# Kernel tuning notes

Hardware: AMD Instinct MI355X
Metric: run time of the kernel (lower is better)

## Reference

```python
import jax, jax.numpy as jnp
import numpy as np

BETA = 2.0  # init kwarg beta


def _roi_map(roi_params, H, W):
    # roi_params: (N, K, 4) = (mu_x, mu_y, sigma_x, sigma_y) in [0, 1]
    dtype = roi_params.dtype
    gx = (jnp.arange(W, dtype=dtype) + 0.5) / W  # x-coords of grid columns
    gy = (jnp.arange(H, dtype=dtype) + 0.5) / H  # y-coords of grid rows
    mu_x, mu_y = roi_params[:, :, 0], roi_params[:, :, 1]
    sg_x, sg_y = roi_params[:, :, 2], roi_params[:, :, 3]
    # separable generalized-Gaussian log pdf along each axis
    log_x = -(jnp.abs(gx[None, None, :] - mu_x[:, :, None]) / sg_x[:, :, None]) ** BETA  # (N,K,W)
    log_y = -(jnp.abs(gy[None, None, :] - mu_y[:, :, None]) / sg_y[:, :, None]) ** BETA  # (N,K,H)
    scores = jnp.exp(log_y[:, :, :, None] + log_x[:, :, None, :])  # (N,K,H,W)
    mx = jnp.max(scores, axis=(2, 3), keepdims=True)
    return scores / (mx + 1e-12)  # max-normalized attention maps


def setup_inputs() -> dict:
    key = jax.random.key(0)
    k1, k2 = jax.random.split(key)
    x = jax.random.normal(k1, (16, 128, 128, 256), dtype=jnp.float32)
    roi_params = jax.random.uniform(k2, (16, 64, 4), dtype=jnp.float32)
    return {"x": x, "roi_params": roi_params}


def reference(x, roi_params):
    N, H, W, d = x.shape
    roi_map = _roi_map(roi_params, H, W)           # (N,K,H,W)
    flat_map = roi_map.reshape(N, -1, H * W)        # (N,K,HW)
    flat_feats = x.reshape(N, H * W, d)             # (N,HW,d)
    roi_features = jnp.einsum('nrf,nfd->nrd', flat_map, flat_feats) / (H * W)
    return roi_features, roi_params, roi_map
```

## Files before the change

kernel.cpp:

```cpp
#include <hip/hip_runtime.h>
#include <hip/hip_bf16.h>
#include <math.h>

#define NB 16
#define RB 64
#define HB 128
#define WB 128
#define DB 256
#define HW (HB * WB)

typedef __attribute__((ext_vector_type(8))) short bf16x8;
typedef __attribute__((ext_vector_type(4))) float f32x4;

static __device__ __forceinline__ short f2bf(float f) {
  __hip_bfloat16 h = __float2bfloat16(f);
  return *reinterpret_cast<short*>(&h);
}

#define GLOAD_LDS16(gp, lp)                                          \
  __builtin_amdgcn_global_load_lds(                                  \
      (const __attribute__((address_space(1))) unsigned int*)(gp),   \
      (__attribute__((address_space(3))) unsigned int*)(lp), 16, 0, 0)

__global__ void tables_kernel(const float* __restrict__ roi,
                              float* __restrict__ ws,
                              float* __restrict__ out_params) {
  const int nr = blockIdx.x;
  const int t  = threadIdx.x;

  const float mux = roi[nr * 4 + 0];
  const float muy = roi[nr * 4 + 1];
  const float sgx = roi[nr * 4 + 2];
  const float sgy = roi[nr * 4 + 3];

  const float g  = (t + 0.5f) * (1.0f / 128.0f);
  const float tx = fabsf(g - mux) / sgx;
  const float ty = fabsf(g - muy) / sgy;
  const float lx = -(tx * tx);
  const float ly = -(ty * ty);

  __shared__ float sdx[128], sdy[128];
  sdx[t] = lx; sdy[t] = ly;
  __syncthreads();
  for (int off = 64; off > 0; off >>= 1) {
    if (t < off) {
      sdx[t] = fmaxf(sdx[t], sdx[t + off]);
      sdy[t] = fmaxf(sdy[t], sdy[t + off]);
    }
    __syncthreads();
  }
  const float mlx = sdx[0], mly = sdy[0];

  const float em = expf(mlx + mly);
  const float s  = em / (em + 1e-12f);
  const float exv = expf(lx - mlx);
  const float eyv = expf(ly - mly) * s;

  float* ex_m = ws;
  float* ey_m = ws + NB * RB * WB;
  ex_m[nr * WB + t] = exv;
  ey_m[nr * HB + t] = eyv;

  if (t < 4) out_params[nr * 4 + t] = roi[nr * 4 + t];
}

__global__ void map_kernel(const float* __restrict__ ws,
                           float* __restrict__ out_map) {
  const float* ex_m = ws;
  const float* ey_m = ws + NB * RB * WB;
  const int total = NB * RB * HB * WB / 4;
  for (int idx = blockIdx.x * blockDim.x + threadIdx.x; idx < total;
       idx += gridDim.x * blockDim.x) {
    const int w4 = idx & 31;
    const int h  = (idx >> 5) & 127;
    const int nr = idx >> 12;
    const float  ey = ey_m[nr * HB + h];
    const float4 ex = *reinterpret_cast<const float4*>(ex_m + nr * WB + w4 * 4);
    float4 o;
    o.x = ey * ex.x; o.y = ey * ex.y; o.z = ey * ex.z; o.w = ey * ex.w;
    reinterpret_cast<float4*>(out_map)[idx] = o;
  }
}

__global__ __launch_bounds__(512, 1) void feat_mfma_kernel(
    const float* __restrict__ x, const float* __restrict__ ws,
    float* __restrict__ partials) {
  __shared__ float buf[4][32 * DB];

  const float* ex_m = ws;
  const float* ey_m = ws + NB * RB * WB;

  const int bid = blockIdx.x;
  const int n   = bid >> 5;
  const int kc  = bid & 31;
  const int t   = threadIdx.x;
  const int l   = t & 63;
  const int wv  = t >> 6;
  const int mh  = wv >> 2;
  const int dw  = wv & 3;
  const int l15 = l & 15;
  const int lk  = (l >> 4) * 8;
  const int h0  = kc * 4;
  const int dbase = dw * 64 + l15 * 4;

  const char* gx =
      (const char*)(x + ((size_t)n * HW + (size_t)kc * 512) * DB);
  char* lbase = (char*)&buf[0][0];

  f32x4 exr[2][4][2];
  float eyv[4][2];
#pragma unroll
  for (int rf = 0; rf < 2; ++rf) {
    const float* exrow =
        ex_m + (size_t)(n * RB + (mh * 2 + rf) * 16 + l15) * WB;
#pragma unroll
    for (int ks = 0; ks < 4; ++ks) {
      exr[rf][ks][0] = *reinterpret_cast<const f32x4*>(exrow + ks * 32 + lk);
      exr[rf][ks][1] = *reinterpret_cast<const f32x4*>(exrow + ks * 32 + lk + 4);
    }
  }
#pragma unroll
  for (int hh = 0; hh < 4; ++hh)
#pragma unroll
    for (int rf = 0; rf < 2; ++rf)
      eyv[hh][rf] =
          ey_m[(size_t)(n * RB + (mh * 2 + rf) * 16 + l15) * HB + h0 + hh];
  asm volatile("s_waitcnt vmcnt(0)" ::: "memory");

  f32x4 acc[2][4];
#pragma unroll
  for (int rf = 0; rf < 2; ++rf)
#pragma unroll
    for (int f = 0; f < 4; ++f) acc[rf][f] = (f32x4)0.0f;

#define STAGE(bi, slot) do {                                                 \
    const char* gsrc_ = gx + (size_t)(bi) * 32768;                           \
    char* ldst_ = lbase + (slot) * 32768;                                    \
    _Pragma("unroll")                                                        \
    for (int ii = 0; ii < 4; ++ii)                                           \
      GLOAD_LDS16(gsrc_ + ii * 8192 + wv * 1024 + l * 16,                    \
                  ldst_ + ii * 8192 + wv * 1024);                            \
  } while (0)

  STAGE(0, 0); STAGE(1, 1); STAGE(2, 2);

#define KSTEP(bi, VM, DO_STAGE) do {                                         \
    asm volatile("s_waitcnt vmcnt(" #VM ")" ::: "memory");                   \
    __builtin_amdgcn_s_barrier();                                            \
    __builtin_amdgcn_sched_barrier(0);                                       \
    if (DO_STAGE) STAGE((bi) + 3, ((bi) + 3) & 3);                           \
    const float* bp_ = &buf[(bi) & 3][0];                                    \
    f32x4 xv_[8];                                                            \
    _Pragma("unroll")                                                        \
    for (int j = 0; j < 8; ++j)                                              \
      xv_[j] = *reinterpret_cast<const f32x4*>(                              \
          bp_ + (lk + j) * DB + dbase);                                      \
    bf16x8 bfr_[4];                                                          \
    _Pragma("unroll")                                                        \
    for (int f = 0; f < 4; ++f) {                                            \
      bf16x8 b_;                                                             \
      _Pragma("unroll")                                                      \
      for (int j = 0; j < 8; ++j) b_[j] = f2bf(xv_[j][f]);                   \
      bfr_[f] = b_;                                                          \
    }                                                                        \
    bf16x8 afr_[2];                                                          \
    _Pragma("unroll")                                                        \
    for (int rf = 0; rf < 2; ++rf) {                                         \
      const float ey_ = eyv[(bi) >> 2][rf];                                  \
      const f32x4 e0_ = exr[rf][(bi) & 3][0];                                \
      const f32x4 e1_ = exr[rf][(bi) & 3][1];                                \
      bf16x8 a_;                                                             \
      a_[0] = f2bf(ey_ * e0_.x); a_[1] = f2bf(ey_ * e0_.y);                  \
      a_[2] = f2bf(ey_ * e0_.z); a_[3] = f2bf(ey_ * e0_.w);                  \
      a_[4] = f2bf(ey_ * e1_.x); a_[5] = f2bf(ey_ * e1_.y);                  \
      a_[6] = f2bf(ey_ * e1_.z); a_[7] = f2bf(ey_ * e1_.w);                  \
      afr_[rf] = a_;                                                         \
    }                                                                        \
    _Pragma("unroll")                                                        \
    for (int rf = 0; rf < 2; ++rf)                                           \
      _Pragma("unroll")                                                      \
      for (int f = 0; f < 4; ++f)                                            \
        acc[rf][f] = __builtin_amdgcn_mfma_f32_16x16x32_bf16(                \
            afr_[rf], bfr_[f], acc[rf][f], 0, 0, 0);                         \
  } while (0)

  KSTEP(0, 8, 1);  KSTEP(1, 8, 1);  KSTEP(2, 8, 1);  KSTEP(3, 8, 1);
  KSTEP(4, 8, 1);  KSTEP(5, 8, 1);  KSTEP(6, 8, 1);  KSTEP(7, 8, 1);
  KSTEP(8, 8, 1);  KSTEP(9, 8, 1);  KSTEP(10, 8, 1); KSTEP(11, 8, 1);
  KSTEP(12, 8, 1); KSTEP(13, 8, 0); KSTEP(14, 4, 0); KSTEP(15, 0, 0);

#undef KSTEP
#undef STAGE

  float* P = partials + (size_t)bid * (RB * DB);
#pragma unroll
  for (int rf = 0; rf < 2; ++rf) {
#pragma unroll
    for (int reg = 0; reg < 4; ++reg) {
      const int r = mh * 32 + rf * 16 + (l >> 4) * 4 + reg;
      f32x4 v;
      v.x = acc[rf][0][reg]; v.y = acc[rf][1][reg];
      v.z = acc[rf][2][reg]; v.w = acc[rf][3][reg];
      *reinterpret_cast<f32x4*>(P + (size_t)r * DB + dbase) = v;
    }
  }
}

__global__ __launch_bounds__(256) void reduce_kernel(
    const float* __restrict__ partials, float* __restrict__ outF) {
  const int idx = blockIdx.x * 256 + threadIdx.x;
  const int n   = idx >> 12;
  const int i4  = idx & 4095;
  const f32x4* p =
      reinterpret_cast<const f32x4*>(partials) + (size_t)n * 32 * 4096 + i4;
  f32x4 s0 = (f32x4)0.0f, s1 = (f32x4)0.0f, s2 = (f32x4)0.0f, s3 = (f32x4)0.0f;
#pragma unroll
  for (int kc = 0; kc < 32; kc += 4) {
    s0 += p[(size_t)(kc + 0) * 4096];
    s1 += p[(size_t)(kc + 1) * 4096];
    s2 += p[(size_t)(kc + 2) * 4096];
    s3 += p[(size_t)(kc + 3) * 4096];
  }
  f32x4 s = (s0 + s1) + (s2 + s3);
  s *= (1.0f / (float)HW);
  reinterpret_cast<f32x4*>(outF)[idx] = s;
}

extern "C" void kernel_launch(void* const* d_in, const int* in_sizes, int n_in,
                              void* d_out, int out_size, void* d_ws, size_t ws_size,
                              hipStream_t stream) {
  const float* x   = (const float*)d_in[0];
  const float* roi = (const float*)d_in[1];
  float* out        = (float*)d_out;
  float* ws         = (float*)d_ws;
  float* out_feat   = out;
  float* out_params = out + NB * RB * DB;
  float* out_map    = out_params + NB * RB * 4;

  const size_t tbl_floats = 2u * NB * RB * WB;
  const size_t par_floats = 512u * RB * DB;
  const bool ws_ok = ws_size >= (tbl_floats + par_floats + 16) * sizeof(float);

  float* P = ws_ok ? (ws + tbl_floats) : out_map;

  tables_kernel<<<NB * RB, 128, 0, stream>>>(roi, ws, out_params);
  feat_mfma_kernel<<<512, 512, 0, stream>>>(x, ws, P);
  reduce_kernel<<<256, 256, 0, stream>>>(P, out_feat);
  map_kernel<<<2048, 256, 0, stream>>>(ws, out_map);
}
```

Baseline: 95.24 us.

## Fuse table generation and map writing into interleaved feature kernel blocks

Removes the separate tables kernel. Each feature block now computes its exp tables inline from roi_params, and the per-axis max is found analytically from the nearest grid point instead of by a shared-memory reduction. The map output is written by extra blocks interleaved with the MFMA blocks in a single launch (every third block), so map stores overlap with the feature GEMM and two launches are dropped. The cost is redundant exp computation in every feature block, and the map blocks still reserve the full 128 KB LDS allocation.

```diff
diff --git a/kernel.cpp b/kernel.cpp
--- a/kernel.cpp
+++ b/kernel.cpp
@@ -22,78 +22,69 @@
       (const __attribute__((address_space(1))) unsigned int*)(gp),   \
       (__attribute__((address_space(3))) unsigned int*)(lp), 16, 0, 0)
 
-__global__ void tables_kernel(const float* __restrict__ roi,
-                              float* __restrict__ ws,
-                              float* __restrict__ out_params) {
-  const int nr = blockIdx.x;
-  const int t  = threadIdx.x;
-
-  const float mux = roi[nr * 4 + 0];
-  const float muy = roi[nr * 4 + 1];
-  const float sgx = roi[nr * 4 + 2];
-  const float sgy = roi[nr * 4 + 3];
-
-  const float g  = (t + 0.5f) * (1.0f / 128.0f);
-  const float tx = fabsf(g - mux) / sgx;
-  const float ty = fabsf(g - muy) / sgy;
-  const float lx = -(tx * tx);
-  const float ly = -(ty * ty);
-
-  __shared__ float sdx[128], sdy[128];
-  sdx[t] = lx; sdy[t] = ly;
-  __syncthreads();
-  for (int off = 64; off > 0; off >>= 1) {
-    if (t < off) {
-      sdx[t] = fmaxf(sdx[t], sdx[t + off]);
-      sdy[t] = fmaxf(sdy[t], sdy[t + off]);
+static __device__ __forceinline__ float axis_maxlog(float mu, float sg) {
+  int i = (int)roundf(mu * 128.0f - 0.5f);
+  i = i < 0 ? 0 : (i > 127 ? 127 : i);
+  const float g = (i + 0.5f) * (1.0f / 128.0f);
+  const float tm = fabsf(g - mu) / sg;
+  return -(tm * tm);
+}
+
+template <bool INTERLEAVE>
+__global__ __launch_bounds__(512, 1) void fused_kernel(
+    const float* __restrict__ x, const float* __restrict__ roi,
+    float* __restrict__ partials, float* __restrict__ out_map,
+    float* __restrict__ out_params) {
+  __shared__ float buf[4][32 * DB];
+
+  const int bid = blockIdx.x;
+  const int t   = threadIdx.x;
+
+  bool is_map = false;
+  int fid = bid, mb = 0;
+  if constexpr (INTERLEAVE) {
+    is_map = (bid % 3) == 2;
+    fid    = (bid / 3) * 2 + (bid % 3);
+    mb     = bid / 3;
+  }
+
+  if (is_map) {
+    float* sEx = &buf[0][0];
+    float* sEy = sEx + 512;
+    for (int v = t; v < 1024; v += 512) {
+      const int rr = v >> 8, axis = (v >> 7) & 1, pos = v & 127;
+      const int nr = mb * 4 + rr;
+      const float4 rp = reinterpret_cast<const float4*>(roi)[nr];
+      const float mlx = axis_maxlog(rp.x, rp.z);
+      const float mly = axis_maxlog(rp.y, rp.w);
+      const float em  = expf(mlx + mly);
+      const float s   = em / (em + 1e-12f);
+      const float g   = (pos + 0.5f) * (1.0f / 128.0f);
+      if (axis == 0) {
+        const float tx = fabsf(g - rp.x) / rp.z;
+        sEx[rr * 128 + pos] = expf(-(tx * tx) - mlx);
+      } else {
+        const float ty = fabsf(g - rp.y) / rp.w;
+        sEy[rr * 128 + pos] = expf(-(ty * ty) - mly) * s;
+      }
+    }
+    if (mb == 0) {
+      for (int i = t; i < NB * RB * 4; i += 512) out_params[i] = roi[i];
     }
     __syncthreads();
-  }
-  const float mlx = sdx[0], mly = sdy[0];
-
-  const float em = expf(mlx + mly);
-  const float s  = em / (em + 1e-12f);
-  const float exv = expf(lx - mlx);
-  const float eyv = expf(ly - mly) * s;
-
-  float* ex_m = ws;
-  float* ey_m = ws + NB * RB * WB;
-  ex_m[nr * WB + t] = exv;
-  ey_m[nr * HB + t] = eyv;
-
-  if (t < 4) out_params[nr * 4 + t] = roi[nr * 4 + t];
-}
-
-__global__ void map_kernel(const float* __restrict__ ws,
-                           float* __restrict__ out_map) {
-  const float* ex_m = ws;
-  const float* ey_m = ws + NB * RB * WB;
-  const int total = NB * RB * HB * WB / 4;
-  for (int idx = blockIdx.x * blockDim.x + threadIdx.x; idx < total;
-       idx += gridDim.x * blockDim.x) {
-    const int w4 = idx & 31;
-    const int h  = (idx >> 5) & 127;
-    const int nr = idx >> 12;
-    const float  ey = ey_m[nr * HB + h];
-    const float4 ex = *reinterpret_cast<const float4*>(ex_m + nr * WB + w4 * 4);
-    float4 o;
-    o.x = ey * ex.x; o.y = ey * ex.y; o.z = ey * ex.z; o.w = ey * ex.w;
-    reinterpret_cast<float4*>(out_map)[idx] = o;
-  }
-}
-
-__global__ __launch_bounds__(512, 1) void feat_mfma_kernel(
-    const float* __restrict__ x, const float* __restrict__ ws,
-    float* __restrict__ partials) {
-  __shared__ float buf[4][32 * DB];
-
-  const float* ex_m = ws;
-  const float* ey_m = ws + NB * RB * WB;
-
-  const int bid = blockIdx.x;
-  const int n   = bid >> 5;
-  const int kc  = bid & 31;
-  const int t   = threadIdx.x;
+    f32x4* dst = reinterpret_cast<f32x4*>(out_map + (size_t)mb * 4 * HW);
+#pragma unroll
+    for (int p = 0; p < 32; ++p) {
+      const int idx = p * 512 + t;
+      const int rr = idx >> 12, h = (idx >> 5) & 127, w4 = idx & 31;
+      const f32x4 e = *reinterpret_cast<const f32x4*>(&sEx[rr * 128 + w4 * 4]);
+      dst[idx] = e * (f32x4)sEy[rr * 128 + h];
+    }
+    return;
+  }
+
+  const int n   = fid >> 5;
+  const int kc  = fid & 31;
   const int l   = t & 63;
   const int wv  = t >> 6;
   const int mh  = wv >> 2;
@@ -111,20 +102,34 @@
   float eyv[4][2];
 #pragma unroll
   for (int rf = 0; rf < 2; ++rf) {
-    const float* exrow =
-        ex_m + (size_t)(n * RB + (mh * 2 + rf) * 16 + l15) * WB;
+    const int nr = n * RB + mh * 32 + rf * 16 + l15;
+    const float4 rp = reinterpret_cast<const float4*>(roi)[nr];
+    const float mlx = axis_maxlog(rp.x, rp.z);
+    const float mly = axis_maxlog(rp.y, rp.w);
+    const float em  = expf(mlx + mly);
+    const float s   = em / (em + 1e-12f);
 #pragma unroll
     for (int ks = 0; ks < 4; ++ks) {
-      exr[rf][ks][0] = *reinterpret_cast<const f32x4*>(exrow + ks * 32 + lk);
-      exr[rf][ks][1] = *reinterpret_cast<const f32x4*>(exrow + ks * 32 + lk + 4);
-    }
-  }
-#pragma unroll
-  for (int hh = 0; hh < 4; ++hh)
-#pragma unroll
-    for (int rf = 0; rf < 2; ++rf)
-      eyv[hh][rf] =
-          ey_m[(size_t)(n * RB + (mh * 2 + rf) * 16 + l15) * HB + h0 + hh];
+#pragma unroll
+      for (int hf = 0; hf < 2; ++hf) {
+        f32x4 v;
+#pragma unroll
+        for (int j = 0; j < 4; ++j) {
+          const int col = ks * 32 + lk + hf * 4 + j;
+          const float g = (col + 0.5f) * (1.0f / 128.0f);
+          const float tx = fabsf(g - rp.x) / rp.z;
+          v[j] = expf(-(tx * tx) - mlx);
+        }
+        exr[rf][ks][hf] = v;
+      }
+    }
+#pragma unroll
+    for (int hh = 0; hh < 4; ++hh) {
+      const float g = (h0 + hh + 0.5f) * (1.0f / 128.0f);
+      const float ty = fabsf(g - rp.y) / rp.w;
+      eyv[hh][rf] = expf(-(ty * ty) - mly) * s;
+    }
+  }
   asm volatile("s_waitcnt vmcnt(0)" ::: "memory");
 
   f32x4 acc[2][4];
@@ -192,7 +197,7 @@
 #undef KSTEP
 #undef STAGE
 
-  float* P = partials + (size_t)bid * (RB * DB);
+  float* P = partials + (size_t)fid * (RB * DB);
 #pragma unroll
   for (int rf = 0; rf < 2; ++rf) {
 #pragma unroll
@@ -203,6 +208,45 @@
       v.z = acc[rf][2][reg]; v.w = acc[rf][3][reg];
       *reinterpret_cast<f32x4*>(P + (size_t)r * DB + dbase) = v;
     }
+  }
+}
+
+__global__ __launch_bounds__(512) void map_only_kernel(
+    const float* __restrict__ roi, float* __restrict__ out_map,
+    float* __restrict__ out_params) {
+  __shared__ float sT[1024];
+  const int mb = blockIdx.x;
+  const int t  = threadIdx.x;
+  float* sEx = sT;
+  float* sEy = sT + 512;
+  for (int v = t; v < 1024; v += 512) {
+    const int rr = v >> 8, axis = (v >> 7) & 1, pos = v & 127;
+    const int nr = mb * 4 + rr;
+    const float4 rp = reinterpret_cast<const float4*>(roi)[nr];
+    const float mlx = axis_maxlog(rp.x, rp.z);
+    const float mly = axis_maxlog(rp.y, rp.w);
+    const float em  = expf(mlx + mly);
+    const float s   = em / (em + 1e-12f);
+    const float g   = (pos + 0.5f) * (1.0f / 128.0f);
+    if (axis == 0) {
+      const float tx = fabsf(g - rp.x) / rp.z;
+      sEx[rr * 128 + pos] = expf(-(tx * tx) - mlx);
+    } else {
+      const float ty = fabsf(g - rp.y) / rp.w;
+      sEy[rr * 128 + pos] = expf(-(ty * ty) - mly) * s;
+    }
+  }
+  if (mb == 0) {
+    for (int i = t; i < NB * RB * 4; i += 512) out_params[i] = roi[i];
+  }
+  __syncthreads();
+  f32x4* dst = reinterpret_cast<f32x4*>(out_map + (size_t)mb * 4 * HW);
+#pragma unroll
+  for (int p = 0; p < 32; ++p) {
+    const int idx = p * 512 + t;
+    const int rr = idx >> 12, h = (idx >> 5) & 127, w4 = idx & 31;
+    const f32x4 e = *reinterpret_cast<const f32x4*>(&sEx[rr * 128 + w4 * 4]);
+    dst[idx] = e * (f32x4)sEy[rr * 128 + h];
   }
 }
 
@@ -237,14 +281,17 @@
   float* out_params = out + NB * RB * DB;
   float* out_map    = out_params + NB * RB * 4;
 
-  const size_t tbl_floats = 2u * NB * RB * WB;
   const size_t par_floats = 512u * RB * DB;
-  const bool ws_ok = ws_size >= (tbl_floats + par_floats + 16) * sizeof(float);
-
-  float* P = ws_ok ? (ws + tbl_floats) : out_map;
-
-  tables_kernel<<<NB * RB, 128, 0, stream>>>(roi, ws, out_params);
-  feat_mfma_kernel<<<512, 512, 0, stream>>>(x, ws, P);
-  reduce_kernel<<<256, 256, 0, stream>>>(P, out_feat);
-  map_kernel<<<2048, 256, 0, stream>>>(ws, out_map);
-}
+  const bool ws_ok = ws_size >= (par_floats + 16) * sizeof(float);
+
+  if (ws_ok) {
+    float* P = ws;
+    fused_kernel<true><<<768, 512, 0, stream>>>(x, roi, P, out_map, out_params);
+    reduce_kernel<<<256, 256, 0, stream>>>(P, out_feat);
+  } else {
+    float* P = out_map;
+    fused_kernel<false><<<512, 512, 0, stream>>>(x, roi, P, out_map, out_params);
+    reduce_kernel<<<256, 256, 0, stream>>>(P, out_feat);
+    map_only_kernel<<<256, 512, 0, stream>>>(roi, out_map, out_params);
+  }
+}
```

Result: slower. 99.12 us (+4.1%).
